# Optimization experiments

Hardware: AMD Instinct MI355X
Metric: run time of the kernel (lower is better)

Reference implementation:

```python
import jax, jax.numpy as jnp
import numpy as np

B, S, H = 2, 2048, 1024
NH, HD = 16, 64  # num heads, head dim


def setup_inputs() -> dict:
    key = jax.random.key(0)
    ks = jax.random.split(key, 8)
    scale = 0.02
    return {
        "hidden_states": jax.random.normal(ks[0], (B, S, H), dtype=jnp.float32),
        "attention_mask": jnp.zeros((B, 1, 1, S), dtype=jnp.float32),
        "Wq": jax.random.normal(ks[1], (H, H), dtype=jnp.float32) * scale,
        "bq": jnp.zeros((H,), dtype=jnp.float32),
        "Wk": jax.random.normal(ks[2], (H, H), dtype=jnp.float32) * scale,
        "bk": jnp.zeros((H,), dtype=jnp.float32),
        "Wv": jax.random.normal(ks[3], (H, H), dtype=jnp.float32) * scale,
        "bv": jnp.zeros((H,), dtype=jnp.float32),
    }


def _split_heads(x):
    # [B,S,H] -> [B,NH,S,HD]
    b, s, _ = x.shape
    return x.reshape(b, s, NH, HD).transpose(0, 2, 1, 3)


def reference(hidden_states, attention_mask, Wq, bq, Wk, bk, Wv, bv):
    q = _split_heads(hidden_states @ Wq.T + bq)
    k = _split_heads(hidden_states @ Wk.T + bk)
    v = _split_heads(hidden_states @ Wv.T + bv)
    # scores: [B,NH,S,S]
    scores = jnp.einsum("bhqd,bhkd->bhqk", q, k) / jnp.sqrt(jnp.float32(HD))
    scores = scores + attention_mask
    att = jax.nn.softmax(scores, axis=-1)  # dropout is identity in eval
    ctx = jnp.einsum("bhqk,bhkd->bhqd", att, v)
    # [B,NH,S,HD] -> [B,S,H]
    return ctx.transpose(0, 2, 1, 3).reshape(hidden_states.shape[0], hidden_states.shape[1], NH * HD)
```

## Files before the change

kernel.cpp:

```cpp
#include <hip/hip_runtime.h>
#include <stdint.h>

#define BB 2
#define SS 2048
#define HH 1024
#define NH 16
#define HD 64

#define LOG2E 1.4426950408889634f
#define QSCALE (0.125f * LOG2E)

typedef short bfrag  __attribute__((ext_vector_type(8)));
typedef short bfrag4 __attribute__((ext_vector_type(4)));
typedef float f32x4  __attribute__((ext_vector_type(4)));

__device__ __forceinline__ short f2bf(float f) {
    union { float f; uint32_t u; } v; v.f = f;
    uint32_t r = (v.u + 0x7fffu + ((v.u >> 16) & 1u)) >> 16;
    return (short)r;
}

__device__ __forceinline__ uint32_t pack_bf16(float a, float b) {
#if __has_builtin(__builtin_amdgcn_cvt_pk_bf16_f32)
    auto t = __builtin_amdgcn_cvt_pk_bf16_f32(a, b);
    uint32_t u; __builtin_memcpy(&u, &t, 4);
    return u;
#else
    uint32_t ua = __float_as_uint(a) + 0x8000u;
    uint32_t ub = __float_as_uint(b) + 0x8000u;
    return __builtin_amdgcn_perm(ub, ua, 0x07060302u);
#endif
}

__global__ __launch_bounds__(256) void cvt_all(
    const float* __restrict__ X,  const float* __restrict__ Wq,
    const float* __restrict__ Wk, const float* __restrict__ Wv,
    const float* __restrict__ mask,
    short* __restrict__ Xb, short* __restrict__ Wcat,
    float* __restrict__ maskl)
{
    int i = blockIdx.x * 256 + threadIdx.x;
    if (i >= 1835008) {
        int off = i - 1835008;
        float4 f = ((const float4*)mask)[off];
        f.x *= LOG2E; f.y *= LOG2E; f.z *= LOG2E; f.w *= LOG2E;
        ((float4*)maskl)[off] = f;
        return;
    }
    const float* src; short* dst; int off;
    if (i < 1048576)      { src = X;  dst = Xb;                 off = i; }
    else if (i < 1310720) { src = Wq; dst = Wcat;               off = i - 1048576; }
    else if (i < 1572864) { src = Wk; dst = Wcat + 1048576;     off = i - 1310720; }
    else                  { src = Wv; dst = Wcat + 2097152;     off = i - 1572864; }
    float4 f = ((const float4*)src)[off];
    short4 s;
    s.x = f2bf(f.x); s.y = f2bf(f.y); s.z = f2bf(f.z); s.w = f2bf(f.w);
    ((short4*)dst)[off] = s;
}

__device__ __forceinline__ void gload_lds16(const void* g, void* lds) {
    __builtin_amdgcn_global_load_lds(
        (__attribute__((address_space(1))) void*)(uintptr_t)g,
        (__attribute__((address_space(3))) void*)(uintptr_t)lds,
        16, 0, 0);
}

__global__ __launch_bounds__(256, 3) void qkv_gemm(
    const short* __restrict__ X, const short* __restrict__ Wcat,
    const float* __restrict__ bq, const float* __restrict__ bk, const float* __restrict__ bv,
    short* __restrict__ Qo, short* __restrict__ Ko, short* __restrict__ Vo)
{
    __shared__ __align__(16) short smem[17408];

    const int tid  = threadIdx.x;
    const int wave = tid >> 6, lane = tid & 63;
    const int quad = lane >> 4, l15 = lane & 15;
    const int mTile = blockIdx.y * 128;
    const int nTile = blockIdx.x * 128;
    const int z = nTile >> 10;
    const int nLocT = nTile & 1023;
    const float* bias = (z == 0) ? bq : (z == 1) ? bk : bv;

    f32x4 acc[4][4];
#pragma unroll
    for (int i = 0; i < 4; ++i)
#pragma unroll
        for (int j = 0; j < 4; ++j) acc[i][j] = (f32x4)0.0f;

    const int srow  = lane >> 3;
    const int c_lin = lane & 7;
    const int mBase = (wave >> 1) * 64;
    const int nBase = (wave & 1) * 64;

    for (int k0 = 0; k0 < 1024; k0 += 64) {
        __syncthreads();
#pragma unroll
        for (int i = 0; i < 4; ++i) {
            int row = i * 32 + wave * 8 + srow;
            int cg  = c_lin ^ (row & 7);
            gload_lds16(X + (size_t)(mTile + row) * 1024 + k0 + cg * 8,
                        (char*)smem + i * 4096 + wave * 1024);
            gload_lds16(Wcat + (size_t)(nTile + row) * 1024 + k0 + cg * 8,
                        (char*)smem + 16384 + i * 4096 + wave * 1024);
        }
        __syncthreads();

#pragma unroll
        for (int kt = 0; kt < 2; ++kt) {
            bfrag af[4], bf[4];
#pragma unroll
            for (int t = 0; t < 4; ++t) {
                int arow = mBase + t * 16 + l15;
                int aslot = (kt * 4 + quad) ^ (arow & 7);
                af[t] = *(const bfrag*)((const char*)smem + arow * 128 + aslot * 16);
                int brow = nBase + t * 16 + l15;
                int bslot = (kt * 4 + quad) ^ (brow & 7);
                bf[t] = *(const bfrag*)((const char*)smem + 16384 + brow * 128 + bslot * 16);
            }
#pragma unroll
            for (int mt = 0; mt < 4; ++mt)
#pragma unroll
                for (int ct = 0; ct < 4; ++ct)
                    acc[mt][ct] = __builtin_amdgcn_mfma_f32_16x16x32_bf16(
                        af[mt], bf[ct], acc[mt][ct], 0, 0, 0);
        }
    }

    __syncthreads();
    const int b = mTile >> 11, sBase = mTile & 2047;

    if (z == 2) {
#pragma unroll
        for (int mt = 0; mt < 4; ++mt)
#pragma unroll
            for (int ct = 0; ct < 4; ++ct)
#pragma unroll
                for (int r = 0; r < 4; ++r) {
                    int nl = nBase + ct * 16 + l15;
                    int sl = mBase + mt * 16 + quad * 4 + r;
                    smem[nl * 136 + sl] = f2bf(acc[mt][ct][r] + bias[nLocT + nl]);
                }
        __syncthreads();
#pragma unroll
        for (int p = 0; p < 8; ++p) {
            int nl = p * 16 + (tid >> 4);
            int cg = tid & 15;
            int blk = cg >> 3;
            int c2  = cg & 7;
            int base = blk * 64 + (c2 >> 2) * 32 + (c2 & 3) * 4;
            int2 lo = *(const int2*)(smem + nl * 136 + base);
            int2 hi = *(const int2*)(smem + nl * 136 + base + 16);
            int4 v; v.x = lo.x; v.y = lo.y; v.z = hi.x; v.w = hi.y;
            int ng = nLocT + nl, hh = ng >> 6, d = ng & 63;
            *(int4*)(Vo + ((size_t)(b * 16 + hh) * 64 + d) * 2048 + sBase + cg * 8) = v;
        }
    } else {
        short* Out = (z == 0) ? Qo : Ko;
        float scale = (z == 0) ? QSCALE : 1.0f;
#pragma unroll
        for (int mt = 0; mt < 4; ++mt)
#pragma unroll
            for (int ct = 0; ct < 4; ++ct)
#pragma unroll
                for (int r = 0; r < 4; ++r) {
                    int ml = mBase + mt * 16 + quad * 4 + r;
                    int nl = nBase + ct * 16 + l15;
                    smem[ml * 136 + nl] = f2bf((acc[mt][ct][r] + bias[nLocT + nl]) * scale);
                }
        __syncthreads();
#pragma unroll
        for (int p = 0; p < 8; ++p) {
            int ml = p * 16 + (tid >> 4);
            int c  = tid & 15;
            bfrag v8 = *(const bfrag*)(smem + ml * 136 + c * 8);
            int s  = sBase + ml;
            int nl = nLocT + c * 8, hh = nl >> 6, d = nl & 63;
            *(bfrag*)(Out + (((size_t)(b * 16 + hh) << 11) + s) * 64 + d) = v8;
        }
    }
}

__global__ __launch_bounds__(128, 2) void attn_kernel(
    const short* __restrict__ Qb, const short* __restrict__ Kb, const short* __restrict__ Vb,
    const float* __restrict__ maskl, float* __restrict__ out)
{
    __shared__ __align__(16) char smem[32768];

    const int tid  = threadIdx.x;
    const int wave = tid >> 6, lane = tid & 63;
    const int quad = lane >> 4, l15 = lane & 15;

    const int id = blockIdx.x;
    const int slot = id >> 3;
    const int bh = ((id & 7) << 2) | (slot & 3);
    const int qt = slot >> 2;
    const int b  = bh >> 4, h = bh & 15;
    const int qBase = qt * 64 + wave * 32;

    int ksrc[4], vsrc[4];
#pragma unroll
    for (int i = 0; i < 4; ++i) {
        int ci = wave * 256 + i * 64 + lane;
        int r = ci >> 3, c = ci & 7;
        int cs = (c ^ (r & 7)) * 16;
        ksrc[i] = r * 128  + cs;
        vsrc[i] = r * 4096 + cs;
    }
    const char* kBase = (const char*)(Kb + (size_t)bh * SS * HD);
    const char* vBase = (const char*)(Vb + (size_t)bh * HD * SS);
    const char* mSrc  = (const char*)(maskl + b * SS) + quad * 16;

    const short* Qp = Qb + ((size_t)bh * SS + qBase) * HD;
    bfrag qf[2][2];
#pragma unroll
    for (int hf = 0; hf < 2; ++hf)
#pragma unroll
        for (int kt = 0; kt < 2; ++kt)
            qf[hf][kt] = *(const bfrag*)(Qp + (size_t)(hf * 16 + l15) * HD + kt * 32 + quad * 8);

    int kAddr[2];
#pragma unroll
    for (int kt = 0; kt < 2; ++kt)
        kAddr[kt] = l15 * 128 + (((kt * 4 + quad) ^ (l15 & 7)) * 16);
    int vAddr[2];
#pragma unroll
    for (int g = 0; g < 2; ++g)
        vAddr[g] = 8192 + l15 * 128 + (((g * 4 + quad) ^ (l15 & 7)) * 16);

    const f32x4 z4 = (f32x4)0.0f;
    const bfrag ones8 = {0x3F80, 0x3F80, 0x3F80, 0x3F80,
                         0x3F80, 0x3F80, 0x3F80, 0x3F80};

    f32x4 oacc[2][4], ol[2];
#pragma unroll
    for (int hf = 0; hf < 2; ++hf) {
        ol[hf] = z4;
#pragma unroll
        for (int dt = 0; dt < 4; ++dt) oacc[hf][dt] = z4;
    }

#pragma unroll
    for (int i = 0; i < 4; ++i) {
        gload_lds16(kBase + ksrc[i], smem + wave * 4096 + i * 1024);
        gload_lds16(vBase + vsrc[i], smem + 8192 + wave * 4096 + i * 1024);
    }

    auto astep = [&](int CUR, int NXT, int jn, int pref) {
        __syncthreads();
        if (pref) {
#pragma unroll
            for (int i = 0; i < 4; ++i) {
                gload_lds16(kBase + (size_t)jn * 8192 + ksrc[i],
                            smem + NXT + wave * 4096 + i * 1024);
                gload_lds16(vBase + (size_t)jn * 128  + vsrc[i],
                            smem + NXT + 8192 + wave * 4096 + i * 1024);
            }
        }

        f32x4 mvl[4];
#pragma unroll
        for (int ct = 0; ct < 4; ++ct)
            mvl[ct] = *(const f32x4*)(mSrc + ct * 64);
        mSrc += 256;

        f32x4 s0[4], s1[4];
        __builtin_amdgcn_s_setprio(1);
#pragma unroll
        for (int ct = 0; ct < 4; ++ct) {
            bfrag kf0 = *(const bfrag*)(smem + CUR + kAddr[0] + ct * 2048);
            bfrag kf1 = *(const bfrag*)(smem + CUR + kAddr[1] + ct * 2048);
            s0[ct] = __builtin_amdgcn_mfma_f32_16x16x32_bf16(kf0, qf[0][0], mvl[ct], 0, 0, 0);
            s0[ct] = __builtin_amdgcn_mfma_f32_16x16x32_bf16(kf1, qf[0][1], s0[ct],  0, 0, 0);
            s1[ct] = __builtin_amdgcn_mfma_f32_16x16x32_bf16(kf0, qf[1][0], mvl[ct], 0, 0, 0);
            s1[ct] = __builtin_amdgcn_mfma_f32_16x16x32_bf16(kf1, qf[1][1], s1[ct],  0, 0, 0);
        }
        __builtin_amdgcn_s_setprio(0);

        bfrag p0[2], p1[2];
#pragma unroll
        for (int g = 0; g < 2; ++g) {
            union { uint32_t u[4]; bfrag v; } cvt;
            cvt.u[0] = pack_bf16(__builtin_amdgcn_exp2f(s0[2*g][0]),   __builtin_amdgcn_exp2f(s0[2*g][1]));
            cvt.u[1] = pack_bf16(__builtin_amdgcn_exp2f(s0[2*g][2]),   __builtin_amdgcn_exp2f(s0[2*g][3]));
            cvt.u[2] = pack_bf16(__builtin_amdgcn_exp2f(s0[2*g+1][0]), __builtin_amdgcn_exp2f(s0[2*g+1][1]));
            cvt.u[3] = pack_bf16(__builtin_amdgcn_exp2f(s0[2*g+1][2]), __builtin_amdgcn_exp2f(s0[2*g+1][3]));
            p0[g] = cvt.v;
            cvt.u[0] = pack_bf16(__builtin_amdgcn_exp2f(s1[2*g][0]),   __builtin_amdgcn_exp2f(s1[2*g][1]));
            cvt.u[1] = pack_bf16(__builtin_amdgcn_exp2f(s1[2*g][2]),   __builtin_amdgcn_exp2f(s1[2*g][3]));
            cvt.u[2] = pack_bf16(__builtin_amdgcn_exp2f(s1[2*g+1][0]), __builtin_amdgcn_exp2f(s1[2*g+1][1]));
            cvt.u[3] = pack_bf16(__builtin_amdgcn_exp2f(s1[2*g+1][2]), __builtin_amdgcn_exp2f(s1[2*g+1][3]));
            p1[g] = cvt.v;
        }

        __builtin_amdgcn_s_setprio(1);
#pragma unroll
        for (int dt = 0; dt < 4; ++dt) {
#pragma unroll
            for (int g = 0; g < 2; ++g) {
                bfrag v = *(const bfrag*)(smem + CUR + vAddr[g] + dt * 2048);
                oacc[0][dt] = __builtin_amdgcn_mfma_f32_16x16x32_bf16(p0[g], v, oacc[0][dt], 0, 0, 0);
                oacc[1][dt] = __builtin_amdgcn_mfma_f32_16x16x32_bf16(p1[g], v, oacc[1][dt], 0, 0, 0);
            }
        }
#pragma unroll
        for (int g = 0; g < 2; ++g) {
            ol[0] = __builtin_amdgcn_mfma_f32_16x16x32_bf16(p0[g], ones8, ol[0], 0, 0, 0);
            ol[1] = __builtin_amdgcn_mfma_f32_16x16x32_bf16(p1[g], ones8, ol[1], 0, 0, 0);
        }
        __builtin_amdgcn_s_setprio(0);
    };

    for (int jj = 0; jj < 16; ++jj) {
        astep(0,     16384, 2 * jj + 1, 1);
        astep(16384, 0,     2 * jj + 2, jj < 15);
    }

#pragma unroll
    for (int hf = 0; hf < 2; ++hf) {
#pragma unroll
        for (int r = 0; r < 4; ++r) {
            float linv = 1.0f / ol[hf][r];
            int qrow = qBase + hf * 16 + quad * 4 + r;
#pragma unroll
            for (int dt = 0; dt < 4; ++dt)
                out[((size_t)(b * SS + qrow)) * HH + h * 64 + dt * 16 + l15] =
                    oacc[hf][dt][r] * linv;
        }
    }
}

extern "C" void kernel_launch(void* const* d_in, const int* in_sizes, int n_in,
                              void* d_out, int out_size, void* d_ws, size_t ws_size,
                              hipStream_t stream) {
    const float* hs   = (const float*)d_in[0];
    const float* mask = (const float*)d_in[1];
    const float* Wq   = (const float*)d_in[2];
    const float* bq   = (const float*)d_in[3];
    const float* Wk   = (const float*)d_in[4];
    const float* bk   = (const float*)d_in[5];
    const float* Wv   = (const float*)d_in[6];
    const float* bv   = (const float*)d_in[7];
    float* out = (float*)d_out;

    char* ws = (char*)d_ws;
    short* Xb    = (short*)(ws);
    short* Wcat  = (short*)(ws + (8ull  << 20));
    short* Qb    = (short*)(ws + (14ull << 20));
    short* Kb    = (short*)(ws + (22ull << 20));
    short* Vb    = (short*)(ws + (30ull << 20));
    float* maskl = (float*)(ws + (38ull << 20));

    cvt_all<<<7172, 256, 0, stream>>>(hs, Wq, Wk, Wv, mask, Xb, Wcat, maskl);

    qkv_gemm<<<dim3(24, 32), 256, 0, stream>>>(Xb, Wcat, bq, bk, bv, Qb, Kb, Vb);

    attn_kernel<<<1024, 128, 0, stream>>>(Qb, Kb, Vb, maskl, out);
}
```

Measured before the change: 162.7 us.

## Drop LDS staging in attention; read K/V fragments directly from global memory

The attention kernel goes from 128-thread blocks that double-buffer K/V tiles through LDS with barriers to single-wave blocks that load MFMA fragments for K and V straight from global memory (through the caches), with 2048 blocks launched. This removes the LDS writes, the __syncthreads and the swizzle bookkeeping, and gives more independent waves. In exchange, every wave re-reads K/V from L2 or global memory with less coalesced 16-byte accesses. The strided V reads (row stride 4 KB) may waste bandwidth, and nothing software-side hides load latency any more.

```diff
diff --git a/kernel.cpp b/kernel.cpp
--- a/kernel.cpp
+++ b/kernel.cpp
@@ -11,7 +11,6 @@
 #define QSCALE (0.125f * LOG2E)
 
 typedef short bfrag  __attribute__((ext_vector_type(8)));
-typedef short bfrag4 __attribute__((ext_vector_type(4)));
 typedef float f32x4  __attribute__((ext_vector_type(4)));
 
 __device__ __forceinline__ short f2bf(float f) {
@@ -180,35 +179,23 @@
     }
 }
 
-__global__ __launch_bounds__(128, 2) void attn_kernel(
+__global__ __launch_bounds__(64) void attn_kernel(
     const short* __restrict__ Qb, const short* __restrict__ Kb, const short* __restrict__ Vb,
     const float* __restrict__ maskl, float* __restrict__ out)
 {
-    __shared__ __align__(16) char smem[32768];
-
-    const int tid  = threadIdx.x;
-    const int wave = tid >> 6, lane = tid & 63;
+    const int lane = threadIdx.x & 63;
     const int quad = lane >> 4, l15 = lane & 15;
 
     const int id = blockIdx.x;
     const int slot = id >> 3;
     const int bh = ((id & 7) << 2) | (slot & 3);
-    const int qt = slot >> 2;
+    const int qw = slot >> 2;
     const int b  = bh >> 4, h = bh & 15;
-    const int qBase = qt * 64 + wave * 32;
-
-    int ksrc[4], vsrc[4];
-#pragma unroll
-    for (int i = 0; i < 4; ++i) {
-        int ci = wave * 256 + i * 64 + lane;
-        int r = ci >> 3, c = ci & 7;
-        int cs = (c ^ (r & 7)) * 16;
-        ksrc[i] = r * 128  + cs;
-        vsrc[i] = r * 4096 + cs;
-    }
-    const char* kBase = (const char*)(Kb + (size_t)bh * SS * HD);
-    const char* vBase = (const char*)(Vb + (size_t)bh * HD * SS);
-    const char* mSrc  = (const char*)(maskl + b * SS) + quad * 16;
+    const int qBase = qw * 32;
+
+    const short* Kp = Kb + (size_t)bh * SS * HD;
+    const short* Vp = Vb + (size_t)bh * HD * SS;
+    const char*  mSrc = (const char*)(maskl + b * SS) + quad * 16;
 
     const short* Qp = Qb + ((size_t)bh * SS + qBase) * HD;
     bfrag qf[2][2];
@@ -217,15 +204,6 @@
 #pragma unroll
         for (int kt = 0; kt < 2; ++kt)
             qf[hf][kt] = *(const bfrag*)(Qp + (size_t)(hf * 16 + l15) * HD + kt * 32 + quad * 8);
-
-    int kAddr[2];
-#pragma unroll
-    for (int kt = 0; kt < 2; ++kt)
-        kAddr[kt] = l15 * 128 + (((kt * 4 + quad) ^ (l15 & 7)) * 16);
-    int vAddr[2];
-#pragma unroll
-    for (int g = 0; g < 2; ++g)
-        vAddr[g] = 8192 + l15 * 128 + (((g * 4 + quad) ^ (l15 & 7)) * 16);
 
     const f32x4 z4 = (f32x4)0.0f;
     const bfrag ones8 = {0x3F80, 0x3F80, 0x3F80, 0x3F80,
@@ -239,36 +217,20 @@
         for (int dt = 0; dt < 4; ++dt) oacc[hf][dt] = z4;
     }
 
-#pragma unroll
-    for (int i = 0; i < 4; ++i) {
-        gload_lds16(kBase + ksrc[i], smem + wave * 4096 + i * 1024);
-        gload_lds16(vBase + vsrc[i], smem + 8192 + wave * 4096 + i * 1024);
-    }
-
-    auto astep = [&](int CUR, int NXT, int jn, int pref) {
-        __syncthreads();
-        if (pref) {
-#pragma unroll
-            for (int i = 0; i < 4; ++i) {
-                gload_lds16(kBase + (size_t)jn * 8192 + ksrc[i],
-                            smem + NXT + wave * 4096 + i * 1024);
-                gload_lds16(vBase + (size_t)jn * 128  + vsrc[i],
-                            smem + NXT + 8192 + wave * 4096 + i * 1024);
-            }
-        }
-
+#pragma unroll 2
+    for (int jn = 0; jn < 32; ++jn) {
         f32x4 mvl[4];
 #pragma unroll
         for (int ct = 0; ct < 4; ++ct)
-            mvl[ct] = *(const f32x4*)(mSrc + ct * 64);
-        mSrc += 256;
+            mvl[ct] = *(const f32x4*)(mSrc + (size_t)jn * 256 + ct * 64);
 
         f32x4 s0[4], s1[4];
         __builtin_amdgcn_s_setprio(1);
 #pragma unroll
         for (int ct = 0; ct < 4; ++ct) {
-            bfrag kf0 = *(const bfrag*)(smem + CUR + kAddr[0] + ct * 2048);
-            bfrag kf1 = *(const bfrag*)(smem + CUR + kAddr[1] + ct * 2048);
+            const short* kr = Kp + (size_t)(jn * 64 + ct * 16 + l15) * 64 + quad * 8;
+            bfrag kf0 = *(const bfrag*)(kr);
+            bfrag kf1 = *(const bfrag*)(kr + 32);
             s0[ct] = __builtin_amdgcn_mfma_f32_16x16x32_bf16(kf0, qf[0][0], mvl[ct], 0, 0, 0);
             s0[ct] = __builtin_amdgcn_mfma_f32_16x16x32_bf16(kf1, qf[0][1], s0[ct],  0, 0, 0);
             s1[ct] = __builtin_amdgcn_mfma_f32_16x16x32_bf16(kf0, qf[1][0], mvl[ct], 0, 0, 0);
@@ -294,25 +256,18 @@
 
         __builtin_amdgcn_s_setprio(1);
 #pragma unroll
-        for (int dt = 0; dt < 4; ++dt) {
-#pragma unroll
-            for (int g = 0; g < 2; ++g) {
-                bfrag v = *(const bfrag*)(smem + CUR + vAddr[g] + dt * 2048);
+        for (int g = 0; g < 2; ++g) {
+#pragma unroll
+            for (int dt = 0; dt < 4; ++dt) {
+                bfrag v = *(const bfrag*)(Vp + (size_t)(dt * 16 + l15) * 2048
+                                             + jn * 64 + (g * 4 + quad) * 8);
                 oacc[0][dt] = __builtin_amdgcn_mfma_f32_16x16x32_bf16(p0[g], v, oacc[0][dt], 0, 0, 0);
                 oacc[1][dt] = __builtin_amdgcn_mfma_f32_16x16x32_bf16(p1[g], v, oacc[1][dt], 0, 0, 0);
             }
-        }
-#pragma unroll
-        for (int g = 0; g < 2; ++g) {
             ol[0] = __builtin_amdgcn_mfma_f32_16x16x32_bf16(p0[g], ones8, ol[0], 0, 0, 0);
             ol[1] = __builtin_amdgcn_mfma_f32_16x16x32_bf16(p1[g], ones8, ol[1], 0, 0, 0);
         }
         __builtin_amdgcn_s_setprio(0);
-    };
-
-    for (int jj = 0; jj < 16; ++jj) {
-        astep(0,     16384, 2 * jj + 1, 1);
-        astep(16384, 0,     2 * jj + 2, jj < 15);
     }
 
 #pragma unroll
@@ -354,5 +309,5 @@
 
     qkv_gemm<<<dim3(24, 32), 256, 0, stream>>>(Xb, Wcat, bq, bk, bv, Qb, Kb, Vb);
 
-    attn_kernel<<<1024, 128, 0, stream>>>(Qb, Kb, Vb, maskl, out);
-}
+    attn_kernel<<<2048, 64, 0, stream>>>(Qb, Kb, Vb, maskl, out);
+}
```

Result: slower. 237.6 us (+46.0%).
